# Optimization experiments

Hardware: AMD Instinct MI355X
Metric: run time of the kernel (lower is better)

## Reference

```python
import jax, jax.numpy as jnp
import numpy as np

NEG_BIG = -1.0e9


def setup_inputs() -> dict:
    key = jax.random.key(0)
    kq, kk, kv, km = jax.random.split(key, 4)
    B, Lq, Lk, D = 16, 2048, 2048, 128
    queries = jax.random.normal(kq, (B, Lq, D), dtype=jnp.float32)
    keys = jax.random.normal(kk, (B, Lk, D), dtype=jnp.float32)
    values = jax.random.normal(kv, (B, Lk, D), dtype=jnp.float32)
    mask = (jax.random.uniform(km, (Lk,)) > 0.8).astype(jnp.float32)
    return {"queries": queries, "keys": keys, "values": values, "mask": mask}


def reference(queries, keys, values, mask):
    d = keys.shape[-1]
    # scores: [B, Lq, Lk]
    scores = jnp.einsum("bqd,bkd->bqk", queries, keys) / jnp.sqrt(jnp.float32(d))
    masked = scores + mask[None, None, :] * NEG_BIG
    attn = jax.nn.softmax(masked, axis=-1)
    # dropout is identity in eval / p=0.0
    return jnp.einsum("bqk,bkd->bqd", attn, values)
```

## Files before the change

### kernel.cpp

```cpp
#include <hip/hip_runtime.h>
#include <hip/hip_bf16.h>


#define B_    16
#define LQ_   2048
#define LK_   2048
#define DIM_  128
#define NTH   256
#define SCALE_ 0.08838834764831845f
#define LOG2E_ 1.4426950408889634f
#define SC2_   (SCALE_ * LOG2E_)
#define MFIX_  12.0f
#define NEGBIG -1.0e9f
#define PS 72

typedef __attribute__((ext_vector_type(8))) short bf16x8;
typedef __attribute__((ext_vector_type(4))) float f32x4;

#define GLDS(gsrc, ldst) \
  __builtin_amdgcn_global_load_lds( \
      (const __attribute__((address_space(1))) unsigned int*)(gsrc), \
      (__attribute__((address_space(3))) unsigned int*)(ldst), 16, 0, 0)

static __device__ __forceinline__ unsigned short f2bf(float f) {
    unsigned int u = __builtin_bit_cast(unsigned int, f);
    u += 0x7fff + ((u >> 16) & 1);
    return (unsigned short)(u >> 16);
}

__global__ __launch_bounds__(NTH) void pack_kv(
    const float* __restrict__ K, const float* __restrict__ V,
    unsigned short* __restrict__ Kb, unsigned short* __restrict__ Vtb)
{
    int bid = blockIdx.x;
    if (bid < 2048) {
        int gid = bid * NTH + threadIdx.x;
        int c = gid & 15, r = (gid >> 4) & 63;
        const float4* s4 = (const float4*)(K + (size_t)gid * 8);
        float4 a = s4[0], bq = s4[1];
        bf16x8 h = { (short)f2bf(a.x),  (short)f2bf(a.y),  (short)f2bf(a.z),  (short)f2bf(a.w),
                     (short)f2bf(bq.x), (short)f2bf(bq.y), (short)f2bf(bq.z), (short)f2bf(bq.w) };
        size_t doff = (size_t)(gid >> 10) * 8192 + r * 128 + ((c ^ (r & 15)) * 8);
        *(bf16x8*)(Kb + doff) = h;
    } else {
        int T = bid - 2048;
        int w = threadIdx.x >> 6, lane = threadIdx.x & 63;
        const float* vb = V + (size_t)T * 64 * DIM_;
        unsigned short* db = Vtb + (size_t)T * 8192;
        #pragma unroll
        for (int half = 0; half < 2; ++half) {
            int d = half * 64 + lane;
            #pragma unroll
            for (int cb = 0; cb < 8; cb += 4) {
                int c = cb + w;
                float v[8];
                #pragma unroll
                for (int kk = 0; kk < 8; ++kk)
                    v[kk] = vb[(size_t)(c * 8 + kk) * DIM_ + d];
                bf16x8 h = { (short)f2bf(v[0]), (short)f2bf(v[1]), (short)f2bf(v[2]), (short)f2bf(v[3]),
                             (short)f2bf(v[4]), (short)f2bf(v[5]), (short)f2bf(v[6]), (short)f2bf(v[7]) };
                *(bf16x8*)(db + d * 64 + ((c ^ (d & 7)) * 8)) = h;
            }
        }
    }
}

__global__ __launch_bounds__(NTH, 2) void attn_mfma3(
    const float* __restrict__ Q, const unsigned short* __restrict__ Kb,
    const unsigned short* __restrict__ Vtb, const float* __restrict__ Mk,
    float* __restrict__ O)
{
    __shared__ __align__(16) char smem[49664];
    unsigned short* sK  = (unsigned short*)(smem);
    unsigned short* sVt = (unsigned short*)(smem + 16384);
    unsigned short* sQ  = (unsigned short*)(smem + 32768);
    unsigned short* sP  = (unsigned short*)(smem + 32768);
    float* sB2 = (float*)(smem + 49152);
    float* sLp = (float*)(smem + 49408);
    float* sO  = (float*)smem;

    const int tid  = threadIdx.x;
    const int w    = tid >> 6, lane = tid & 63;
    const int quad = lane >> 4, l15 = lane & 15;
    const int rg   = (w & 1) * 32;
    const int wh   = w >> 1;
    const int kh   = wh * 32;

    const int bid = blockIdx.x;
    const int grp = bid >> 3;
    const int b   = (bid & 7) + 8 * (grp & 1);
    const int q0  = (grp >> 1) * 64;

    {
        const float4* Qg = (const float4*)(Q + ((size_t)b * LQ_ + q0) * DIM_);
        #pragma unroll
        for (int it = 0; it < 8; ++it) {
            int i = tid + it * NTH;
            int r = i >> 5, c4 = i & 31;
            float4 v = Qg[r * 32 + c4];
            ushort4 h = { f2bf(v.x), f2bf(v.y), f2bf(v.z), f2bf(v.w) };
            *(ushort4*)&sQ[r * 128 + (((c4 >> 1) ^ (r & 15)) * 8) + (c4 & 1) * 4] = h;
        }
    }
    __syncthreads();

    bf16x8 aQ[2][4];
    #pragma unroll
    for (int rs = 0; rs < 2; ++rs)
        #pragma unroll
        for (int ks = 0; ks < 4; ++ks)
            aQ[rs][ks] = *(const bf16x8*)&sQ[(rg + rs * 16 + l15) * 128 +
                                             (((ks * 4 + quad) ^ l15) * 8)];

    float l_i[2][4];
    f32x4 acc[2][8];
    #pragma unroll
    for (int rs = 0; rs < 2; ++rs) {
        #pragma unroll
        for (int r = 0; r < 4; ++r) l_i[rs][r] = 0.f;
        #pragma unroll
        for (int dt = 0; dt < 8; ++dt) acc[rs][dt] = (f32x4){0.f, 0.f, 0.f, 0.f};
    }

    for (int k0 = 0; k0 < LK_; k0 += 64) {
        __syncthreads();

        const char* ksrc = (const char*)Kb  + (size_t)(b * 32 + (k0 >> 6)) * 16384;
        const char* vsrc = (const char*)Vtb + (size_t)(b * 32 + (k0 >> 6)) * 16384;
        #pragma unroll
        for (int j = 0; j < 4; ++j) {
            int o = (j * 4 + w) * 1024;
            GLDS(ksrc + o + lane * 16, smem + o);
            GLDS(vsrc + o + lane * 16, smem + 16384 + o);
        }
        if (tid < 64) sB2[tid] = (Mk[k0 + tid] * NEGBIG - MFIX_) * LOG2E_;
        __syncthreads();

        f32x4 s_[2][2];
        #pragma unroll
        for (int kt2 = 0; kt2 < 2; ++kt2) {
            f32x4 c0 = (f32x4){0.f, 0.f, 0.f, 0.f};
            f32x4 c1 = (f32x4){0.f, 0.f, 0.f, 0.f};
            #pragma unroll
            for (int ks = 0; ks < 4; ++ks) {
                bf16x8 bk = *(const bf16x8*)&sK[(kh + kt2 * 16 + l15) * 128 +
                                                (((ks * 4 + quad) ^ l15) * 8)];
                c0 = __builtin_amdgcn_mfma_f32_16x16x32_bf16(aQ[0][ks], bk, c0, 0, 0, 0);
                c1 = __builtin_amdgcn_mfma_f32_16x16x32_bf16(aQ[1][ks], bk, c1, 0, 0, 0);
            }
            float bias = sB2[kh + kt2 * 16 + l15];
            #pragma unroll
            for (int r = 0; r < 4; ++r) {
                s_[0][kt2][r] = c0[r] * SC2_ + bias;
                s_[1][kt2][r] = c1[r] * SC2_ + bias;
            }
        }

        #pragma unroll
        for (int rs = 0; rs < 2; ++rs) {
            #pragma unroll
            for (int r = 0; r < 4; ++r) {
                float p0 = exp2f(s_[rs][0][r]);
                float p1 = exp2f(s_[rs][1][r]);
                int row = rg + rs * 16 + quad * 4 + r;
                sP[row * PS + kh + l15]      = f2bf(p0);
                sP[row * PS + kh + 16 + l15] = f2bf(p1);
                float v = p0 + p1;
                #pragma unroll
                for (int off = 1; off < 16; off <<= 1) v += __shfl_xor(v, off);
                l_i[rs][r] += v;
            }
        }

        bf16x8 aP0 = *(const bf16x8*)&sP[(rg + l15) * PS + kh + quad * 8];
        bf16x8 aP1 = *(const bf16x8*)&sP[(rg + 16 + l15) * PS + kh + quad * 8];
        #pragma unroll
        for (int dt = 0; dt < 8; ++dt) {
            int d = dt * 16 + l15;
            bf16x8 bv = *(const bf16x8*)&sVt[d * 64 + (((wh * 4 + quad) ^ (l15 & 7)) * 8)];
            acc[0][dt] = __builtin_amdgcn_mfma_f32_16x16x32_bf16(aP0, bv, acc[0][dt], 0, 0, 0);
            acc[1][dt] = __builtin_amdgcn_mfma_f32_16x16x32_bf16(aP1, bv, acc[1][dt], 0, 0, 0);
        }
    }

    __syncthreads();
    if (wh == 1) {
        #pragma unroll
        for (int rs = 0; rs < 2; ++rs) {
            #pragma unroll
            for (int r = 0; r < 4; ++r) {
                int row = rg + rs * 16 + quad * 4 + r;
                #pragma unroll
                for (int dt = 0; dt < 8; ++dt)
                    sO[row * 128 + dt * 16 + l15] = acc[rs][dt][r];
                if (l15 == 0) sLp[row] = l_i[rs][r];
            }
        }
    }
    __syncthreads();
    if (wh == 0) {
        float* Og = O + ((size_t)b * LQ_ + q0) * DIM_;
        #pragma unroll
        for (int rs = 0; rs < 2; ++rs) {
            #pragma unroll
            for (int r = 0; r < 4; ++r) {
                int row = rg + rs * 16 + quad * 4 + r;
                float inv = 1.0f / (l_i[rs][r] + sLp[row]);
                #pragma unroll
                for (int dt = 0; dt < 8; ++dt)
                    Og[(size_t)row * DIM_ + dt * 16 + l15] =
                        (acc[rs][dt][r] + sO[row * 128 + dt * 16 + l15]) * inv;
            }
        }
    }
}

#define QS 136
#define VS 72
__global__ __launch_bounds__(NTH, 2) void attn_fallback(
    const float* __restrict__ Q, const float* __restrict__ K,
    const float* __restrict__ V, const float* __restrict__ Mk,
    float* __restrict__ O)
{
    __shared__ __align__(16) unsigned short sQ[64][QS];
    __shared__ __align__(16) unsigned short sK[64][QS];
    __shared__ __align__(16) unsigned short sVt[DIM_][VS];
    __shared__ __align__(16) unsigned short sP[64][VS];
    __shared__ float sB[64];

    const int tid  = threadIdx.x;
    const int w    = tid >> 6, lane = tid & 63;
    const int quad = lane >> 4, l15 = lane & 15;
    const int bid = blockIdx.x;
    const int grp = bid >> 3;
    const int b   = (bid & 7) + 8 * (grp & 1);
    const int q0  = (grp >> 1) * 64;

    {
        const float4* Qg = (const float4*)(Q + ((size_t)b * LQ_ + q0) * DIM_);
        #pragma unroll
        for (int it = 0; it < 8; ++it) {
            int i = tid + it * NTH;
            int r = i >> 5, c4 = i & 31;
            float4 v = Qg[r * 32 + c4];
            ushort4 h = { f2bf(v.x), f2bf(v.y), f2bf(v.z), f2bf(v.w) };
            *(ushort4*)&sQ[r][c4 * 4] = h;
        }
    }
    __syncthreads();
    bf16x8 aQ[4];
    #pragma unroll
    for (int ks = 0; ks < 4; ++ks)
        aQ[ks] = *(const bf16x8*)&sQ[w * 16 + l15][ks * 32 + quad * 8];

    float m_i[4], l_i[4];
    f32x4 acc[8];
    #pragma unroll
    for (int r = 0; r < 4; ++r) { m_i[r] = -3.0e38f; l_i[r] = 0.f; }
    #pragma unroll
    for (int dt = 0; dt < 8; ++dt) acc[dt] = (f32x4){0.f, 0.f, 0.f, 0.f};

    for (int k0 = 0; k0 < LK_; k0 += 64) {
        const float4* Kg = (const float4*)(K + ((size_t)b * LK_ + k0) * DIM_);
        const float4* Vg = (const float4*)(V + ((size_t)b * LK_ + k0) * DIM_);
        #pragma unroll
        for (int it = 0; it < 8; ++it) {
            int i = tid + it * NTH;
            int r = i >> 5, c4 = i & 31;
            float4 kv = Kg[r * 32 + c4];
            ushort4 h = { f2bf(kv.x), f2bf(kv.y), f2bf(kv.z), f2bf(kv.w) };
            *(ushort4*)&sK[r][c4 * 4] = h;
            float4 vv = Vg[r * 32 + c4];
            int d = c4 * 4;
            sVt[d + 0][r] = f2bf(vv.x);
            sVt[d + 1][r] = f2bf(vv.y);
            sVt[d + 2][r] = f2bf(vv.z);
            sVt[d + 3][r] = f2bf(vv.w);
        }
        if (tid < 64) sB[tid] = Mk[k0 + tid] * NEGBIG;
        __syncthreads();

        f32x4 s[4];
        #pragma unroll
        for (int kt = 0; kt < 4; ++kt) {
            f32x4 c = (f32x4){0.f, 0.f, 0.f, 0.f};
            #pragma unroll
            for (int ks = 0; ks < 4; ++ks) {
                bf16x8 bk = *(const bf16x8*)&sK[kt * 16 + l15][ks * 32 + quad * 8];
                c = __builtin_amdgcn_mfma_f32_16x16x32_bf16(aQ[ks], bk, c, 0, 0, 0);
            }
            float bias = sB[kt * 16 + l15];
            #pragma unroll
            for (int r = 0; r < 4; ++r) s[kt][r] = c[r] * SCALE_ + bias;
        }
        #pragma unroll
        for (int r = 0; r < 4; ++r) {
            float mx = fmaxf(fmaxf(s[0][r], s[1][r]), fmaxf(s[2][r], s[3][r]));
            #pragma unroll
            for (int off = 1; off < 16; off <<= 1) mx = fmaxf(mx, __shfl_xor(mx, off));
            float mn = fmaxf(m_i[r], mx);
            float al = __expf(m_i[r] - mn);
            m_i[r] = mn;
            float rsum = 0.f;
            #pragma unroll
            for (int kt = 0; kt < 4; ++kt) {
                float p = __expf(s[kt][r] - mn);
                rsum += p;
                sP[w * 16 + quad * 4 + r][kt * 16 + l15] = f2bf(p);
            }
            #pragma unroll
            for (int off = 1; off < 16; off <<= 1) rsum += __shfl_xor(rsum, off);
            l_i[r] = l_i[r] * al + rsum;
            #pragma unroll
            for (int dt = 0; dt < 8; ++dt) acc[dt][r] *= al;
        }
        bf16x8 aP0 = *(const bf16x8*)&sP[w * 16 + l15][quad * 8];
        bf16x8 aP1 = *(const bf16x8*)&sP[w * 16 + l15][32 + quad * 8];
        #pragma unroll
        for (int dt = 0; dt < 8; ++dt) {
            bf16x8 bv0 = *(const bf16x8*)&sVt[dt * 16 + l15][quad * 8];
            bf16x8 bv1 = *(const bf16x8*)&sVt[dt * 16 + l15][32 + quad * 8];
            acc[dt] = __builtin_amdgcn_mfma_f32_16x16x32_bf16(aP0, bv0, acc[dt], 0, 0, 0);
            acc[dt] = __builtin_amdgcn_mfma_f32_16x16x32_bf16(aP1, bv1, acc[dt], 0, 0, 0);
        }
        __syncthreads();
    }
    float* Og = O + ((size_t)b * LQ_ + q0 + w * 16) * DIM_;
    #pragma unroll
    for (int r = 0; r < 4; ++r) {
        float inv = 1.0f / l_i[r];
        int row = quad * 4 + r;
        #pragma unroll
        for (int dt = 0; dt < 8; ++dt)
            Og[(size_t)row * DIM_ + dt * 16 + l15] = acc[dt][r] * inv;
    }
}

extern "C" void kernel_launch(void* const* d_in, const int* in_sizes, int n_in,
                              void* d_out, int out_size, void* d_ws, size_t ws_size,
                              hipStream_t stream)
{
    const float* Q  = (const float*)d_in[0];
    const float* K  = (const float*)d_in[1];
    const float* V  = (const float*)d_in[2];
    const float* Mk = (const float*)d_in[3];
    float* O = (float*)d_out;

    const size_t seg = (size_t)B_ * LK_ * DIM_ * 2;
    if (ws_size >= 2 * seg) {
        unsigned short* Kb  = (unsigned short*)d_ws;
        unsigned short* Vtb = Kb + seg / 2;
        hipLaunchKernelGGL(pack_kv, dim3(2560), dim3(NTH), 0, stream, K, V, Kb, Vtb);
        hipLaunchKernelGGL(attn_mfma3, dim3(512), dim3(NTH), 0, stream, Q, Kb, Vtb, Mk, O);
    } else {
        hipLaunchKernelGGL(attn_fallback, dim3(512), dim3(NTH), 0, stream, Q, K, V, Mk, O);
    }
}
```

Baseline: 171.7 us.

## Double-buffer K/V tiles in LDS and compute row sums via MFMA with ones

Splits the K and V^T shared-memory tiles into two buffers so the async global-to-LDS load of the next tile overlaps compute on the current one, cutting each iteration from two barriers to one. Row sums of P are now accumulated by an extra MFMA against a vector of bf16 ones instead of shuffle reductions. Q staging is done in two halves through the P buffer to fit LDS. LDS use grows to about 75KB, which may limit occupancy to fewer than the intended two blocks per CU, and the row sums now come from bf16-rounded P.

```diff
diff --git a/kernel.cpp b/kernel.cpp
--- a/kernel.cpp
+++ b/kernel.cpp
@@ -65,19 +65,18 @@
     }
 }
 
-__global__ __launch_bounds__(NTH, 2) void attn_mfma3(
+__global__ __launch_bounds__(NTH, 2) void attn_mfma4(
     const float* __restrict__ Q, const unsigned short* __restrict__ Kb,
     const unsigned short* __restrict__ Vtb, const float* __restrict__ Mk,
     float* __restrict__ O)
 {
-    __shared__ __align__(16) char smem[49664];
-    unsigned short* sK  = (unsigned short*)(smem);
-    unsigned short* sVt = (unsigned short*)(smem + 16384);
-    unsigned short* sQ  = (unsigned short*)(smem + 32768);
-    unsigned short* sP  = (unsigned short*)(smem + 32768);
-    float* sB2 = (float*)(smem + 49152);
-    float* sLp = (float*)(smem + 49408);
-    float* sO  = (float*)smem;
+    __shared__ __align__(16) unsigned short sKa[8192];
+    __shared__ __align__(16) unsigned short sVta[8192];
+    __shared__ __align__(16) unsigned short sKb_[8192];
+    __shared__ __align__(16) unsigned short sVtb_[8192];
+    __shared__ __align__(16) unsigned short sP[64 * PS];
+    __shared__ float sB2[2 * 64];
+    __shared__ float sLp[64];
 
     const int tid  = threadIdx.x;
     const int w    = tid >> 6, lane = tid & 63;
@@ -91,127 +90,148 @@
     const int b   = (bid & 7) + 8 * (grp & 1);
     const int q0  = (grp >> 1) * 64;
 
+    bf16x8 vone;
+    #pragma unroll
+    for (int j = 0; j < 8; ++j) vone[j] = (short)0x3F80;
+
+    bf16x8 aQ[2][4];
     {
         const float4* Qg = (const float4*)(Q + ((size_t)b * LQ_ + q0) * DIM_);
         #pragma unroll
-        for (int it = 0; it < 8; ++it) {
-            int i = tid + it * NTH;
-            int r = i >> 5, c4 = i & 31;
-            float4 v = Qg[r * 32 + c4];
-            ushort4 h = { f2bf(v.x), f2bf(v.y), f2bf(v.z), f2bf(v.w) };
-            *(ushort4*)&sQ[r * 128 + (((c4 >> 1) ^ (r & 15)) * 8) + (c4 & 1) * 4] = h;
-        }
-    }
-    __syncthreads();
-
-    bf16x8 aQ[2][4];
-    #pragma unroll
-    for (int rs = 0; rs < 2; ++rs)
-        #pragma unroll
-        for (int ks = 0; ks < 4; ++ks)
-            aQ[rs][ks] = *(const bf16x8*)&sQ[(rg + rs * 16 + l15) * 128 +
-                                             (((ks * 4 + quad) ^ l15) * 8)];
-
-    float l_i[2][4];
-    f32x4 acc[2][8];
-    #pragma unroll
-    for (int rs = 0; rs < 2; ++rs) {
-        #pragma unroll
-        for (int r = 0; r < 4; ++r) l_i[rs][r] = 0.f;
-        #pragma unroll
-        for (int dt = 0; dt < 8; ++dt) acc[rs][dt] = (f32x4){0.f, 0.f, 0.f, 0.f};
-    }
-
-    for (int k0 = 0; k0 < LK_; k0 += 64) {
-        __syncthreads();
-
-        const char* ksrc = (const char*)Kb  + (size_t)(b * 32 + (k0 >> 6)) * 16384;
-        const char* vsrc = (const char*)Vtb + (size_t)(b * 32 + (k0 >> 6)) * 16384;
+        for (int h = 0; h < 2; ++h) {
+            #pragma unroll
+            for (int it = 0; it < 4; ++it) {
+                int i2 = tid + it * NTH;
+                int r = i2 >> 5, c4 = i2 & 31;
+                float4 v = Qg[(h * 32 + r) * 32 + c4];
+                ushort4 hh = { f2bf(v.x), f2bf(v.y), f2bf(v.z), f2bf(v.w) };
+                *(ushort4*)&sP[r * 128 + (((c4 >> 1) ^ (r & 15)) * 8) + (c4 & 1) * 4] = hh;
+            }
+            __syncthreads();
+            if ((rg >> 5) == h) {
+                #pragma unroll
+                for (int rs = 0; rs < 2; ++rs)
+                    #pragma unroll
+                    for (int ks = 0; ks < 4; ++ks)
+                        aQ[rs][ks] = *(const bf16x8*)&sP[(rs * 16 + l15) * 128 +
+                                                         (((ks * 4 + quad) ^ l15) * 8)];
+            }
+            __syncthreads();
+        }
+    }
+
+    {
+        const char* ksrc = (const char*)Kb  + (size_t)(b * 32) * 16384;
+        const char* vsrc = (const char*)Vtb + (size_t)(b * 32) * 16384;
         #pragma unroll
         for (int j = 0; j < 4; ++j) {
             int o = (j * 4 + w) * 1024;
-            GLDS(ksrc + o + lane * 16, smem + o);
-            GLDS(vsrc + o + lane * 16, smem + 16384 + o);
-        }
-        if (tid < 64) sB2[tid] = (Mk[k0 + tid] * NEGBIG - MFIX_) * LOG2E_;
-        __syncthreads();
-
-        f32x4 s_[2][2];
-        #pragma unroll
-        for (int kt2 = 0; kt2 < 2; ++kt2) {
-            f32x4 c0 = (f32x4){0.f, 0.f, 0.f, 0.f};
-            f32x4 c1 = (f32x4){0.f, 0.f, 0.f, 0.f};
-            #pragma unroll
-            for (int ks = 0; ks < 4; ++ks) {
-                bf16x8 bk = *(const bf16x8*)&sK[(kh + kt2 * 16 + l15) * 128 +
-                                                (((ks * 4 + quad) ^ l15) * 8)];
-                c0 = __builtin_amdgcn_mfma_f32_16x16x32_bf16(aQ[0][ks], bk, c0, 0, 0, 0);
-                c1 = __builtin_amdgcn_mfma_f32_16x16x32_bf16(aQ[1][ks], bk, c1, 0, 0, 0);
-            }
-            float bias = sB2[kh + kt2 * 16 + l15];
+            GLDS(ksrc + o + lane * 16, (char*)sKa + o);
+            GLDS(vsrc + o + lane * 16, (char*)sVta + o);
+        }
+        if (tid < 64) sB2[tid] = (Mk[tid] * NEGBIG - MFIX_) * LOG2E_;
+    }
+    __syncthreads();
+
+    f32x4 acc[2][8], lacc[2];
+    #pragma unroll
+    for (int rs = 0; rs < 2; ++rs) {
+        lacc[rs] = (f32x4){0.f, 0.f, 0.f, 0.f};
+        #pragma unroll
+        for (int dt = 0; dt < 8; ++dt) acc[rs][dt] = (f32x4){0.f, 0.f, 0.f, 0.f};
+    }
+
+#define TILE_BODY(CURK, CURV, NXTK, NXTV, I) do {                              \
+    const int nxt = (I) + 1;                                                   \
+    if (nxt < 32) {                                                            \
+        const char* ksrc = (const char*)Kb  + (size_t)(b * 32 + nxt) * 16384;  \
+        const char* vsrc = (const char*)Vtb + (size_t)(b * 32 + nxt) * 16384;  \
+        _Pragma("unroll")                                                      \
+        for (int j = 0; j < 4; ++j) {                                          \
+            int o = (j * 4 + w) * 1024;                                        \
+            GLDS(ksrc + o + lane * 16, (char*)(NXTK) + o);                     \
+            GLDS(vsrc + o + lane * 16, (char*)(NXTV) + o);                     \
+        }                                                                      \
+        if (tid < 64)                                                          \
+            sB2[(nxt & 1) * 64 + tid] =                                        \
+                (Mk[nxt * 64 + tid] * NEGBIG - MFIX_) * LOG2E_;                \
+    }                                                                          \
+    f32x4 s_[2][2];                                                            \
+    _Pragma("unroll")                                                          \
+    for (int kt2 = 0; kt2 < 2; ++kt2) {                                        \
+        f32x4 c0 = (f32x4){0.f,0.f,0.f,0.f}, c1 = (f32x4){0.f,0.f,0.f,0.f};   \
+        _Pragma("unroll")                                                      \
+        for (int ks = 0; ks < 4; ++ks) {                                       \
+            bf16x8 bk = *(const bf16x8*)&(CURK)[(kh + kt2 * 16 + l15) * 128 +  \
+                                                (((ks * 4 + quad) ^ l15) * 8)];\
+            c0 = __builtin_amdgcn_mfma_f32_16x16x32_bf16(aQ[0][ks], bk, c0, 0,0,0); \
+            c1 = __builtin_amdgcn_mfma_f32_16x16x32_bf16(aQ[1][ks], bk, c1, 0,0,0); \
+        }                                                                      \
+        float bias = sB2[((I) & 1) * 64 + kh + kt2 * 16 + l15];                \
+        _Pragma("unroll")                                                      \
+        for (int r = 0; r < 4; ++r) {                                          \
+            s_[0][kt2][r] = c0[r] * SC2_ + bias;                               \
+            s_[1][kt2][r] = c1[r] * SC2_ + bias;                               \
+        }                                                                      \
+    }                                                                          \
+    _Pragma("unroll")                                                          \
+    for (int rs = 0; rs < 2; ++rs)                                             \
+        _Pragma("unroll")                                                      \
+        for (int r = 0; r < 4; ++r) {                                          \
+            int row = rg + rs * 16 + quad * 4 + r;                             \
+            sP[row * PS + kh + l15]      = f2bf(exp2f(s_[rs][0][r]));          \
+            sP[row * PS + kh + 16 + l15] = f2bf(exp2f(s_[rs][1][r]));          \
+        }                                                                      \
+    {                                                                          \
+        bf16x8 aP0 = *(const bf16x8*)&sP[(rg + l15) * PS + kh + quad * 8];     \
+        bf16x8 aP1 = *(const bf16x8*)&sP[(rg + 16 + l15) * PS + kh + quad * 8];\
+        lacc[0] = __builtin_amdgcn_mfma_f32_16x16x32_bf16(aP0, vone, lacc[0], 0,0,0); \
+        lacc[1] = __builtin_amdgcn_mfma_f32_16x16x32_bf16(aP1, vone, lacc[1], 0,0,0); \
+        _Pragma("unroll")                                                      \
+        for (int dt = 0; dt < 8; ++dt) {                                       \
+            int d = dt * 16 + l15;                                             \
+            bf16x8 bv = *(const bf16x8*)&(CURV)[d * 64 +                       \
+                                        (((wh * 4 + quad) ^ (l15 & 7)) * 8)];  \
+            acc[0][dt] = __builtin_amdgcn_mfma_f32_16x16x32_bf16(aP0, bv, acc[0][dt], 0,0,0); \
+            acc[1][dt] = __builtin_amdgcn_mfma_f32_16x16x32_bf16(aP1, bv, acc[1][dt], 0,0,0); \
+        }                                                                      \
+    }                                                                          \
+    __syncthreads();                                                           \
+} while (0)
+
+    for (int kk = 0; kk < 32; kk += 2) {
+        TILE_BODY(sKa,  sVta,  sKb_, sVtb_, kk);
+        TILE_BODY(sKb_, sVtb_, sKa,  sVta,  kk + 1);
+    }
+#undef TILE_BODY
+
+    float* sOw = (rg == 0) ? (float*)sKa : (float*)sVta;
+    if (wh == 1) {
+        #pragma unroll
+        for (int rs = 0; rs < 2; ++rs)
             #pragma unroll
             for (int r = 0; r < 4; ++r) {
-                s_[0][kt2][r] = c0[r] * SC2_ + bias;
-                s_[1][kt2][r] = c1[r] * SC2_ + bias;
-            }
-        }
-
-        #pragma unroll
-        for (int rs = 0; rs < 2; ++rs) {
-            #pragma unroll
-            for (int r = 0; r < 4; ++r) {
-                float p0 = exp2f(s_[rs][0][r]);
-                float p1 = exp2f(s_[rs][1][r]);
-                int row = rg + rs * 16 + quad * 4 + r;
-                sP[row * PS + kh + l15]      = f2bf(p0);
-                sP[row * PS + kh + 16 + l15] = f2bf(p1);
-                float v = p0 + p1;
-                #pragma unroll
-                for (int off = 1; off < 16; off <<= 1) v += __shfl_xor(v, off);
-                l_i[rs][r] += v;
-            }
-        }
-
-        bf16x8 aP0 = *(const bf16x8*)&sP[(rg + l15) * PS + kh + quad * 8];
-        bf16x8 aP1 = *(const bf16x8*)&sP[(rg + 16 + l15) * PS + kh + quad * 8];
-        #pragma unroll
-        for (int dt = 0; dt < 8; ++dt) {
-            int d = dt * 16 + l15;
-            bf16x8 bv = *(const bf16x8*)&sVt[d * 64 + (((wh * 4 + quad) ^ (l15 & 7)) * 8)];
-            acc[0][dt] = __builtin_amdgcn_mfma_f32_16x16x32_bf16(aP0, bv, acc[0][dt], 0, 0, 0);
-            acc[1][dt] = __builtin_amdgcn_mfma_f32_16x16x32_bf16(aP1, bv, acc[1][dt], 0, 0, 0);
-        }
-    }
-
-    __syncthreads();
-    if (wh == 1) {
-        #pragma unroll
-        for (int rs = 0; rs < 2; ++rs) {
-            #pragma unroll
-            for (int r = 0; r < 4; ++r) {
-                int row = rg + rs * 16 + quad * 4 + r;
+                int lrow = rs * 16 + quad * 4 + r;
                 #pragma unroll
                 for (int dt = 0; dt < 8; ++dt)
-                    sO[row * 128 + dt * 16 + l15] = acc[rs][dt][r];
-                if (l15 == 0) sLp[row] = l_i[rs][r];
-            }
-        }
+                    sOw[lrow * 128 + dt * 16 + l15] = acc[rs][dt][r];
+                if (l15 == 0) sLp[rg + lrow] = lacc[rs][r];
+            }
     }
     __syncthreads();
     if (wh == 0) {
-        float* Og = O + ((size_t)b * LQ_ + q0) * DIM_;
-        #pragma unroll
-        for (int rs = 0; rs < 2; ++rs) {
+        float* Og = O + ((size_t)b * LQ_ + q0 + rg) * DIM_;
+        #pragma unroll
+        for (int rs = 0; rs < 2; ++rs)
             #pragma unroll
             for (int r = 0; r < 4; ++r) {
-                int row = rg + rs * 16 + quad * 4 + r;
-                float inv = 1.0f / (l_i[rs][r] + sLp[row]);
+                int lrow = rs * 16 + quad * 4 + r;
+                float inv = 1.0f / (lacc[rs][r] + sLp[rg + lrow]);
                 #pragma unroll
                 for (int dt = 0; dt < 8; ++dt)
-                    Og[(size_t)row * DIM_ + dt * 16 + l15] =
-                        (acc[rs][dt][r] + sO[row * 128 + dt * 16 + l15]) * inv;
-            }
-        }
+                    Og[(size_t)lrow * DIM_ + dt * 16 + l15] =
+                        (acc[rs][dt][r] + sOw[lrow * 128 + dt * 16 + l15]) * inv;
+            }
     }
 }
 
@@ -225,7 +245,7 @@
     __shared__ __align__(16) unsigned short sQ[64][QS];
     __shared__ __align__(16) unsigned short sK[64][QS];
     __shared__ __align__(16) unsigned short sVt[DIM_][VS];
-    __shared__ __align__(16) unsigned short sP[64][VS];
+    __shared__ __align__(16) unsigned short sPf[64][VS];
     __shared__ float sB[64];
 
     const int tid  = threadIdx.x;
@@ -306,7 +326,7 @@
             for (int kt = 0; kt < 4; ++kt) {
                 float p = __expf(s[kt][r] - mn);
                 rsum += p;
-                sP[w * 16 + quad * 4 + r][kt * 16 + l15] = f2bf(p);
+                sPf[w * 16 + quad * 4 + r][kt * 16 + l15] = f2bf(p);
             }
             #pragma unroll
             for (int off = 1; off < 16; off <<= 1) rsum += __shfl_xor(rsum, off);
@@ -314,8 +334,8 @@
             #pragma unroll
             for (int dt = 0; dt < 8; ++dt) acc[dt][r] *= al;
         }
-        bf16x8 aP0 = *(const bf16x8*)&sP[w * 16 + l15][quad * 8];
-        bf16x8 aP1 = *(const bf16x8*)&sP[w * 16 + l15][32 + quad * 8];
+        bf16x8 aP0 = *(const bf16x8*)&sPf[w * 16 + l15][quad * 8];
+        bf16x8 aP1 = *(const bf16x8*)&sPf[w * 16 + l15][32 + quad * 8];
         #pragma unroll
         for (int dt = 0; dt < 8; ++dt) {
             bf16x8 bv0 = *(const bf16x8*)&sVt[dt * 16 + l15][quad * 8];
@@ -351,7 +371,7 @@
         unsigned short* Kb  = (unsigned short*)d_ws;
         unsigned short* Vtb = Kb + seg / 2;
         hipLaunchKernelGGL(pack_kv, dim3(2560), dim3(NTH), 0, stream, K, V, Kb, Vtb);
-        hipLaunchKernelGGL(attn_mfma3, dim3(512), dim3(NTH), 0, stream, Q, Kb, Vtb, Mk, O);
+        hipLaunchKernelGGL(attn_mfma4, dim3(512), dim3(NTH), 0, stream, Q, Kb, Vtb, Mk, O);
     } else {
         hipLaunchKernelGGL(attn_fallback, dim3(512), dim3(NTH), 0, stream, Q, K, V, Mk, O);
     }
```

Result: faster. 157.2 us (-8.4%).
